# Kernel tuning notes

Hardware: AMD Instinct MI355X
Metric: run time of the kernel (lower is better)

Reference implementation:

```python
import jax, jax.numpy as jnp
import numpy as np

B = 256          # number of trees
DEPTH = 8        # complete binary tree depth -> 9 levels
M = 2 ** (DEPTH + 1) - 1   # 511 nodes per tree
N = B * M        # 130816 total nodes
X_SIZE = 128
H_SIZE = 128


def _build_forest():
    j = np.arange(M)
    parent_local = np.maximum((j - 1) // 2, 0)
    lvl = np.array([int(x + 1).bit_length() - 1 for x in j], dtype=np.int32)
    off = (np.arange(B) * M).astype(np.int32)
    parent = (parent_local[None, :] + off[:, None]).reshape(-1).astype(np.int32)
    level = np.tile(lvl, B)
    tree_id = np.repeat(np.arange(B, dtype=np.int32), M)
    isleaf = (level == DEPTH)
    jj = j[1:]
    edge_src = (jj[None, :] + off[:, None]).reshape(-1).astype(np.int32)   # child
    edge_dst = parent[edge_src]                                            # parent
    return parent, level, tree_id, isleaf, edge_src, edge_dst, off


def setup_inputs() -> dict:
    key = jax.random.key(0)
    ks = jax.random.split(key, 12)
    _, level, tree_id, isleaf, edge_src, edge_dst, root_ids = _build_forest()
    sx = 1.0 / np.sqrt(X_SIZE)
    sh = 1.0 / np.sqrt(H_SIZE)
    sxh = 1.0 / np.sqrt(X_SIZE + H_SIZE)
    inp = {
        "X": jax.random.normal(ks[0], (N, X_SIZE), dtype=jnp.float32),
        "h0": jnp.zeros((N, H_SIZE), jnp.float32),
        "c0": jnp.zeros((N, H_SIZE), jnp.float32),
        # bottom-up cell params
        "W_iou_bu": jax.random.normal(ks[1], (3 * H_SIZE, X_SIZE), dtype=jnp.float32) * sx,
        "U_iou_bu": jax.random.normal(ks[2], (3 * H_SIZE, H_SIZE), dtype=jnp.float32) * sh,
        "b_iou_bu": jnp.zeros((1, 3 * H_SIZE), jnp.float32),
        "Uf_bu": jax.random.normal(ks[3], (H_SIZE, H_SIZE), dtype=jnp.float32) * sh,
        "bf_bu": jax.random.normal(ks[4], (H_SIZE,), dtype=jnp.float32) * sh,
        # top-down cell params (x_size = X_SIZE + H_SIZE)
        "W_iou_td": jax.random.normal(ks[5], (3 * H_SIZE, X_SIZE + H_SIZE), dtype=jnp.float32) * sxh,
        "U_iou_td": jax.random.normal(ks[6], (3 * H_SIZE, H_SIZE), dtype=jnp.float32) * sh,
        "b_iou_td": jnp.zeros((1, 3 * H_SIZE), jnp.float32),
        "Uf_td": jax.random.normal(ks[7], (H_SIZE, H_SIZE), dtype=jnp.float32) * sh,
        "bf_td": jax.random.normal(ks[8], (H_SIZE,), dtype=jnp.float32) * sh,
        # graph structure
        "edge_src": jnp.asarray(edge_src),
        "edge_dst": jnp.asarray(edge_dst),
        "level": jnp.asarray(level),
        "tree_id": jnp.asarray(tree_id),
        "isleaf": jnp.asarray(isleaf),
        "root_ids": jnp.asarray(root_ids),
    }
    return inp


def _propagate(X_in, W_iou, U_iou, b_iou, Uf, bf, src, dst, level, no_in, h0, c0, order):
    """Level-synchronous ChildSum TreeLSTM propagation (== dgl.prop_nodes_topo)."""
    n = X_in.shape[0]
    WX = X_in @ W_iou.T                                   # [N, 3H]
    h, c = h0, c0
    for t in order:
        h_src = h[src]                                    # [E, H] gather child/parent states
        c_src = c[src]
        h_tild = jax.ops.segment_sum(h_src, dst, num_segments=n)
        f = jax.nn.sigmoid(h_src @ Uf.T + bf)             # per-edge forget gate
        c_red = jax.ops.segment_sum(f * c_src, dst, num_segments=n)
        iou = WX + h_tild @ U_iou.T + b_iou
        i, o, u = jnp.split(iou, 3, axis=1)
        c_base = jnp.where(no_in[:, None], c0, c_red)     # frontier nodes with no in-edges keep init c
        c_new = jax.nn.sigmoid(i) * jnp.tanh(u) + c_base
        h_new = jax.nn.sigmoid(o) * jnp.tanh(c_new)
        m = (level == t)[:, None]                          # only commit current topological level
        h = jnp.where(m, h_new, h)
        c = jnp.where(m, c_new, c)
    return h


def reference(X, h0, c0, W_iou_bu, U_iou_bu, b_iou_bu, Uf_bu, bf_bu,
              W_iou_td, U_iou_td, b_iou_td, Uf_td, bf_td,
              edge_src, edge_dst, level, tree_id, isleaf, root_ids):
    # bottom-up: messages flow child -> parent, leaves first
    h_bu = _propagate(X, W_iou_bu, U_iou_bu, b_iou_bu, Uf_bu, bf_bu,
                      edge_src, edge_dst, level, isleaf, h0, c0,
                      order=range(DEPTH, -1, -1))
    # top-down: reversed edges, root first
    X_td = jnp.concatenate([X, h_bu], axis=1)
    h_td = _propagate(X_td, W_iou_td, U_iou_td, b_iou_td, Uf_td, bf_td,
                      edge_dst, edge_src, level, level == 0, h0, c0,
                      order=range(0, DEPTH + 1))
    root_h_bottom_up = h_bu[root_ids]                     # [B, H]
    leaf = isleaf.astype(h_td.dtype)
    sums = jax.ops.segment_sum(h_td * leaf[:, None], tree_id, num_segments=root_ids.shape[0])
    cnt = jax.ops.segment_sum(leaf, tree_id, num_segments=root_ids.shape[0])
    leaves_h_top_down = sums / cnt[:, None]               # per-tree mean over leaves
    return jnp.concatenate([root_h_bottom_up, leaves_h_top_down], axis=1)
```

## Files before the change

### kernel.cpp

```cpp
#include <hip/hip_runtime.h>
#include <cmath>

#define NTREE 256
#define MPT 511
#define NNODE (NTREE * MPT)
#define HS 128

typedef __bf16 bf16x8 __attribute__((ext_vector_type(8)));
typedef float  f32x4  __attribute__((ext_vector_type(4)));

__device__ __forceinline__ float sigf(float x) {
  float e = __builtin_amdgcn_exp2f(x * -1.44269504f);
  return __builtin_amdgcn_rcpf(1.0f + e);
}
__device__ __forceinline__ float tanh_fast(float x) {
  float e = __builtin_amdgcn_exp2f(x * -2.88539008f);
  return __builtin_amdgcn_rcpf(1.0f + e) * 2.0f - 1.0f;
}
__device__ __forceinline__ f32x4 mm(bf16x8 a, bf16x8 b, f32x4 c) {
  return __builtin_amdgcn_mfma_f32_16x16x32_bf16(a, b, c, 0, 0, 0);
}
__device__ __forceinline__ int swz(int row, int rb, int kb) { return row * rb + (kb ^ ((row & 7) << 4)); }
__device__ __forceinline__ void st8(char* s, int row, int rb, int chunk, bf16x8 v) {
  *reinterpret_cast<bf16x8*>(s + swz(row, rb, chunk * 16)) = v;
}
__device__ __forceinline__ bf16x8 ld8(const char* s, int row, int rb, int kb) {
  return *reinterpret_cast<const bf16x8*>(s + swz(row, rb, kb));
}
__device__ __forceinline__ bf16x8 g8(const __bf16* p) { return *reinterpret_cast<const bf16x8*>(p); }
__device__ __forceinline__ bf16x8 gx8(const float* p) {
  float4 v0 = reinterpret_cast<const float4*>(p)[0];
  float4 v1 = reinterpret_cast<const float4*>(p)[1];
  bf16x8 o;
  o[0] = (__bf16)v0.x; o[1] = (__bf16)v0.y; o[2] = (__bf16)v0.z; o[3] = (__bf16)v0.w;
  o[4] = (__bf16)v1.x; o[5] = (__bf16)v1.y; o[6] = (__bf16)v1.z; o[7] = (__bf16)v1.w;
  return o;
}
__device__ __forceinline__ void stbf(char* s, int row, int rb, int kbyte, float v) {
  *reinterpret_cast<__bf16*>(s + row * rb + (kbyte ^ ((row & 7) << 4))) = (__bf16)v;
}

template <int MODE, bool EPI>
__global__ void __launch_bounds__(512, 2)
level_big8(int t,
           const float*  __restrict__ Xf,
           const __bf16* __restrict__ W,
           const float*  __restrict__ bp,
           const __bf16* __restrict__ Uf,
           const float*  __restrict__ bf_,
           __bf16* __restrict__ h_bu,
           __bf16* __restrict__ h_td,
           float*  __restrict__ cws,
           float*  __restrict__ part)
{
  constexpr int KA = (MODE == 0) ? 128 : 384;
  constexpr int KS = KA / 32;
  constexpr int BK = (MODE == 3) ? 384 : 256;
  constexpr int RB = KA * 2;
  constexpr int HB = (MODE == 0) ? 0 : 512;
  constexpr bool LEAFOUT = (MODE == 3 && !EPI);

  __shared__ __align__(16) char sA[64 * RB];
  __shared__ int sG[64], sP[64];

  const int tid = threadIdx.x;
  const int w = tid >> 6, l = tid & 63, lr = l & 15, lk = l >> 4;
  const int ch = w * 16 + lr;

  if (tid < 64) {
    int v = blockIdx.x * 64 + tid;
    int b = v >> t;
    int j = (1 << t) - 1 + (v & ((1 << t) - 1));
    sG[tid] = b * MPT + j;
    sP[tid] = b * MPT + ((j - 1) >> 1);
  }
  __syncthreads();

  bf16x8 Wr[KS][3];
#pragma unroll
  for (int ks = 0; ks < KS; ++ks)
#pragma unroll
    for (int g2 = 0; g2 < 3; ++g2)
      Wr[ks][g2] = g8(W + (size_t)(g2 * 128 + ch) * BK + ks * 32 + lk * 8);

#pragma unroll
  for (int it = 0; it < 2; ++it) {
    int idx = tid + it * 512, n = idx >> 4, e = idx & 15;
    st8(sA, n, RB, e, gx8(Xf + (size_t)sG[n] * HS + e * 8));
  }
  if constexpr (MODE == 3) {
#pragma unroll
    for (int it = 0; it < 2; ++it) {
      int idx = tid + it * 512, n = idx >> 4, e = idx & 15;
      st8(sA, n, RB, 16 + e, g8(h_bu + (size_t)sG[n] * HS + e * 8));
    }
#pragma unroll
    for (int it = 0; it < 2; ++it) {
      int idx = tid + it * 512, n = idx >> 4, e = idx & 15;
      st8(sA, n, RB, 32 + e, g8(h_td + (size_t)sP[n] * HS + e * 8));
    }
  }
  __syncthreads();

  float cb[4][4];
  const float bia = bp[ch], boa = bp[ch + 128], bua = bp[ch + 256];
  float bfa = 0.0f;
  if constexpr (EPI) bfa = bf_[ch];
  if constexpr (MODE == 3) {
#pragma unroll
    for (int mf = 0; mf < 4; ++mf)
#pragma unroll
      for (int j = 0; j < 4; ++j)
        cb[mf][j] = cws[(size_t)sP[16 * mf + lk * 4 + j] * HS + ch];
  }

  f32x4 acc[3][4];
#pragma unroll
  for (int g2 = 0; g2 < 3; ++g2)
#pragma unroll
    for (int mf = 0; mf < 4; ++mf) acc[g2][mf] = 0.0f;

#pragma unroll
  for (int ks = 0; ks < KS; ++ks) {
    bf16x8 A0 = ld8(sA, lr,      RB, ks * 64 + lk * 16);
    bf16x8 A1 = ld8(sA, 16 + lr, RB, ks * 64 + lk * 16);
    bf16x8 A2 = ld8(sA, 32 + lr, RB, ks * 64 + lk * 16);
    bf16x8 A3 = ld8(sA, 48 + lr, RB, ks * 64 + lk * 16);
#pragma unroll
    for (int g2 = 0; g2 < 3; ++g2) {
      acc[g2][0] = mm(A0, Wr[ks][g2], acc[g2][0]);
      acc[g2][1] = mm(A1, Wr[ks][g2], acc[g2][1]);
      acc[g2][2] = mm(A2, Wr[ks][g2], acc[g2][2]);
      acc[g2][3] = mm(A3, Wr[ks][g2], acc[g2][3]);
    }
  }

  float cnv[4][4], hnv[4][4];
  float psum = 0.0f;
#pragma unroll
  for (int mf = 0; mf < 4; ++mf)
#pragma unroll
    for (int j = 0; j < 4; ++j) {
      const int nrow = 16 * mf + lk * 4 + j;
      float cbase = (MODE == 0) ? 0.0f : cb[mf][j];
      float cn = sigf(acc[0][mf][j] + bia) * tanh_fast(acc[2][mf][j] + bua) + cbase;
      float hn = sigf(acc[1][mf][j] + boa) * tanh_fast(cn);
      if constexpr (!LEAFOUT)
        ((MODE == 3) ? h_td : h_bu)[(size_t)sG[nrow] * HS + ch] = (__bf16)hn;
      if constexpr (EPI) { cnv[mf][j] = cn; hnv[mf][j] = hn; }
      if constexpr (LEAFOUT) psum += hn;
    }

  if constexpr (LEAFOUT) {
    float s = psum;
    s += __shfl_xor(s, 16);
    s += __shfl_xor(s, 32);
    if (lk == 0) part[(size_t)blockIdx.x * 128 + ch] = s;
  }

  if constexpr (EPI) {
    bf16x8 Uff[4];
#pragma unroll
    for (int ks = 0; ks < 4; ++ks)
      Uff[ks] = g8(Uf + (size_t)ch * HS + ks * 32 + lk * 8);
    __syncthreads();
#pragma unroll
    for (int mf = 0; mf < 4; ++mf)
#pragma unroll
      for (int j = 0; j < 4; ++j)
        stbf(sA, 16 * mf + lk * 4 + j, RB, HB + 2 * ch, hnv[mf][j]);
    __syncthreads();
    f32x4 fa[4];
#pragma unroll
    for (int mf = 0; mf < 4; ++mf) fa[mf] = 0.0f;
#pragma unroll
    for (int ks = 0; ks < 4; ++ks) {
      bf16x8 a0 = ld8(sA, lr,      RB, HB + ks * 64 + lk * 16);
      bf16x8 a1 = ld8(sA, 16 + lr, RB, HB + ks * 64 + lk * 16);
      bf16x8 a2 = ld8(sA, 32 + lr, RB, HB + ks * 64 + lk * 16);
      bf16x8 a3 = ld8(sA, 48 + lr, RB, HB + ks * 64 + lk * 16);
      fa[0] = mm(a0, Uff[ks], fa[0]);
      fa[1] = mm(a1, Uff[ks], fa[1]);
      fa[2] = mm(a2, Uff[ks], fa[2]);
      fa[3] = mm(a3, Uff[ks], fa[3]);
    }
#pragma unroll
    for (int mf = 0; mf < 4; ++mf)
#pragma unroll
      for (int p = 0; p < 2; ++p) {
        const int er = 16 * mf + lk * 4 + 2 * p;
        float f0 = sigf(fa[mf][2 * p]     + bfa) * cnv[mf][2 * p];
        float f1 = sigf(fa[mf][2 * p + 1] + bfa) * cnv[mf][2 * p + 1];
        const int gp = sP[er];
        cws[(size_t)gp * HS + ch] = f0 + f1;
        h_bu[(size_t)gp * HS + ch] = (__bf16)(hnv[mf][2 * p] + hnv[mf][2 * p + 1]);
      }
  }
}

template <int MODE>
__global__ void __launch_bounds__(256, 2)
level_big(int t,
          const float*  __restrict__ Xf,
          const __bf16* __restrict__ W,
          const float*  __restrict__ bp,
          const __bf16* __restrict__ Uf,
          const float*  __restrict__ bf_,
          __bf16* __restrict__ h_bu,
          __bf16* __restrict__ h_td,
          float*  __restrict__ cws)
{
  constexpr int KA = (MODE == 1) ? 256 : 384;
  constexpr int KS = KA / 32;
  constexpr int BK = (MODE == 3) ? 384 : 256;
  constexpr int RB = KA * 2;
  constexpr int HB = (MODE == 1) ? 256 : 512;

  __shared__ __align__(16) char sA[64 * RB];
  __shared__ int sG[64], sP[64];

  const int tid = threadIdx.x;
  const int w = tid >> 6, l = tid & 63, lr = l & 15, lk = l >> 4;

  if (tid < 64) {
    int v = blockIdx.x * 64 + tid;
    int b = v >> t;
    int j = (1 << t) - 1 + (v & ((1 << t) - 1));
    sG[tid] = b * MPT + j;
    sP[tid] = b * MPT + ((j - 1) >> 1);
  }
  __syncthreads();

#pragma unroll
  for (int it = 0; it < 4; ++it) {
    int idx = tid + it * 256, n = idx >> 4, e = idx & 15;
    st8(sA, n, RB, e, gx8(Xf + (size_t)sG[n] * HS + e * 8));
  }
#pragma unroll
  for (int it = 0; it < 4; ++it) {
    int idx = tid + it * 256, n = idx >> 4, e = idx & 15;
    st8(sA, n, RB, 16 + e, g8(h_bu + (size_t)sG[n] * HS + e * 8));
  }
  if constexpr (MODE == 3) {
#pragma unroll
    for (int it = 0; it < 4; ++it) {
      int idx = tid + it * 256, n = idx >> 4, e = idx & 15;
      st8(sA, n, RB, 32 + e, g8(h_td + (size_t)sP[n] * HS + e * 8));
    }
  }
  __syncthreads();

  float cb[2][4][4];
  float bia[2], boa[2], bua[2], bfa[2];
#pragma unroll
  for (int nf = 0; nf < 2; ++nf) {
    const int ch = w * 32 + nf * 16 + lr;
    bia[nf] = bp[ch]; boa[nf] = bp[ch + 128]; bua[nf] = bp[ch + 256];
    bfa[nf] = bf_[ch];
#pragma unroll
    for (int mf = 0; mf < 4; ++mf)
#pragma unroll
      for (int j = 0; j < 4; ++j) {
        const int nrow = 16 * mf + lk * 4 + j;
        const int src = (MODE == 1) ? sG[nrow] : sP[nrow];
        cb[nf][mf][j] = cws[(size_t)src * HS + ch];
      }
  }

  f32x4 acc[6][4];
#pragma unroll
  for (int p = 0; p < 6; ++p)
#pragma unroll
    for (int mf = 0; mf < 4; ++mf) acc[p][mf] = 0.0f;

  bf16x8 A0[4], A1[4], Bb[3][6];
  auto ldA = [&](int ks, bf16x8* Ad) {
#pragma unroll
    for (int mf = 0; mf < 4; ++mf) Ad[mf] = ld8(sA, mf * 16 + lr, RB, ks * 64 + lk * 16);
  };
  auto ldB = [&](int ks, int s) {
#pragma unroll
    for (int g2 = 0; g2 < 3; ++g2)
#pragma unroll
      for (int nf = 0; nf < 2; ++nf)
        Bb[s][g2 * 2 + nf] = g8(W + (size_t)(g2 * 128 + w * 32 + nf * 16 + lr) * BK + ks * 32 + lk * 8);
  };

  ldB(0, 0); ldA(0, A0); ldB(1, 1);
#pragma unroll
  for (int ks = 0; ks < KS; ++ks) {
    bf16x8* Ac = (ks & 1) ? A1 : A0;
    bf16x8* An = (ks & 1) ? A0 : A1;
    if (ks + 1 < KS) ldA(ks + 1, An);
    if (ks + 2 < KS) ldB(ks + 2, (ks + 2) % 3);
#pragma unroll
    for (int p = 0; p < 6; ++p)
#pragma unroll
      for (int mf = 0; mf < 4; ++mf) acc[p][mf] = mm(Ac[mf], Bb[ks % 3][p], acc[p][mf]);
  }

  bf16x8 Uff[8];
#pragma unroll
  for (int ks = 0; ks < 4; ++ks)
#pragma unroll
    for (int nf = 0; nf < 2; ++nf)
      Uff[ks * 2 + nf] = g8(Uf + (size_t)(w * 32 + nf * 16 + lr) * HS + ks * 32 + lk * 8);

  __bf16* hp = (MODE == 3) ? h_td : h_bu;
  float cnv[2][4][4], hnv[2][4][4];
#pragma unroll
  for (int nf = 0; nf < 2; ++nf) {
    const int ch = w * 32 + nf * 16 + lr;
#pragma unroll
    for (int mf = 0; mf < 4; ++mf)
#pragma unroll
      for (int j = 0; j < 4; ++j) {
        const int nrow = 16 * mf + lk * 4 + j;
        float cn = sigf(acc[nf][mf][j] + bia[nf]) * tanh_fast(acc[4 + nf][mf][j] + bua[nf]) + cb[nf][mf][j];
        float hn = sigf(acc[2 + nf][mf][j] + boa[nf]) * tanh_fast(cn);
        hp[(size_t)sG[nrow] * HS + ch] = (__bf16)hn;
        cnv[nf][mf][j] = cn; hnv[nf][mf][j] = hn;
      }
  }

  __syncthreads();
#pragma unroll
  for (int nf = 0; nf < 2; ++nf) {
    const int ch = w * 32 + nf * 16 + lr;
#pragma unroll
    for (int mf = 0; mf < 4; ++mf)
#pragma unroll
      for (int j = 0; j < 4; ++j)
        stbf(sA, 16 * mf + lk * 4 + j, RB, HB + 2 * ch, hnv[nf][mf][j]);
  }
  __syncthreads();
  f32x4 fa[4][2];
#pragma unroll
  for (int mf = 0; mf < 4; ++mf) { fa[mf][0] = 0.0f; fa[mf][1] = 0.0f; }
#pragma unroll
  for (int ks = 0; ks < 4; ++ks) {
    bf16x8 a0 = ld8(sA, lr,      RB, HB + ks * 64 + lk * 16);
    bf16x8 a1 = ld8(sA, 16 + lr, RB, HB + ks * 64 + lk * 16);
    bf16x8 a2 = ld8(sA, 32 + lr, RB, HB + ks * 64 + lk * 16);
    bf16x8 a3 = ld8(sA, 48 + lr, RB, HB + ks * 64 + lk * 16);
#pragma unroll
    for (int nf = 0; nf < 2; ++nf) {
      fa[0][nf] = mm(a0, Uff[ks * 2 + nf], fa[0][nf]);
      fa[1][nf] = mm(a1, Uff[ks * 2 + nf], fa[1][nf]);
      fa[2][nf] = mm(a2, Uff[ks * 2 + nf], fa[2][nf]);
      fa[3][nf] = mm(a3, Uff[ks * 2 + nf], fa[3][nf]);
    }
  }
#pragma unroll
  for (int nf = 0; nf < 2; ++nf) {
    const int ch = w * 32 + nf * 16 + lr;
    if constexpr (MODE == 3) {
#pragma unroll
      for (int mf = 0; mf < 4; ++mf)
#pragma unroll
        for (int j = 0; j < 4; ++j) {
          const int nrow = 16 * mf + lk * 4 + j;
          cws[(size_t)sG[nrow] * HS + ch] = sigf(fa[mf][nf][j] + bfa[nf]) * cnv[nf][mf][j];
        }
    } else {
#pragma unroll
      for (int mf = 0; mf < 4; ++mf)
#pragma unroll
        for (int p = 0; p < 2; ++p) {
          const int er = 16 * mf + lk * 4 + 2 * p;
          float f0 = sigf(fa[mf][nf][2 * p]     + bfa[nf]) * cnv[nf][mf][2 * p];
          float f1 = sigf(fa[mf][nf][2 * p + 1] + bfa[nf]) * cnv[nf][mf][2 * p + 1];
          const int gp = sP[er];
          cws[(size_t)gp * HS + ch] = f0 + f1;
          h_bu[(size_t)gp * HS + ch] = (__bf16)(hnv[nf][mf][2 * p] + hnv[nf][mf][2 * p + 1]);
        }
    }
  }
}

__global__ void __launch_bounds__(512, 2)
small_both(const float* __restrict__ Xf,
           const __bf16* __restrict__ Wbu, const float* __restrict__ bbu,
           const __bf16* __restrict__ Ufb, const float* __restrict__ bfb,
           const __bf16* __restrict__ Wtd, const float* __restrict__ btd,
           const __bf16* __restrict__ Uft, const float* __restrict__ bft,
           __bf16* __restrict__ h_bu, __bf16* __restrict__ h_td,
           float* __restrict__ cws)
{
  __shared__ __align__(16) char sX[31 * 256];
  __shared__ __align__(16) char sH[31 * 256];
  __shared__ __align__(16) char sT[16 * 256];
  __shared__ __align__(16) char sTd[15 * 256];
  __shared__ float sCr[16][128];
  __shared__ float sFc[16][128];

  const int tid = threadIdx.x, w = tid >> 6, l = tid & 63, lr = l & 15, lk = l >> 4;
  const int ch = w * 16 + lr;
  const size_t base = (size_t)blockIdx.x * MPT * HS;

  for (int idx = tid; idx < 31 * 16; idx += 512) {
    int n = idx >> 4, e = idx & 15;
    st8(sX, n, 256, e, gx8(Xf + base + (size_t)n * HS + e * 8));
  }
  if (tid < 256) { int n = tid >> 4, e = tid & 15;
    st8(sT, n, 256, e, g8(h_bu + base + (size_t)(15 + n) * HS + e * 8)); }
  { int n = tid >> 5, e = tid & 31;
    reinterpret_cast<float4*>(&sCr[n][0])[e] =
        reinterpret_cast<const float4*>(cws + base + (size_t)(15 + n) * HS)[e]; }
  for (int idx = tid; idx < 15 * 16; idx += 512)
    *reinterpret_cast<float4*>(sTd + idx * 16) = float4{0.f, 0.f, 0.f, 0.f};

  {
    const float bia = bbu[ch], boa = bbu[ch + 128], bua = bbu[ch + 256], bfa = bfb[ch];
    bf16x8 Wb[8][3], Uff[4];
#pragma unroll
    for (int ks = 0; ks < 8; ++ks)
#pragma unroll
      for (int g2 = 0; g2 < 3; ++g2)
        Wb[ks][g2] = g8(Wbu + (size_t)(g2 * 128 + ch) * 256 + ks * 32 + lk * 8);
#pragma unroll
    for (int ks = 0; ks < 4; ++ks)
      Uff[ks] = g8(Ufb + (size_t)ch * HS + ks * 32 + lk * 8);
    __syncthreads();

    for (int t = 4; t >= 0; --t) {
      const int cnt = 1 << t, j0 = cnt - 1;
      f32x4 acc0 = 0.0f, acc1 = 0.0f, acc2 = 0.0f;
      bf16x8 Aa[3];
      auto ldA = [&](int ks, int s) {
        const int kb = (ks & 3) * 64 + lk * 16;
        Aa[s] = (ks < 4) ? ld8(sX, j0 + lr, 256, kb) : ld8(sT, lr, 256, kb);
      };
      ldA(0, 0); ldA(1, 1);
#pragma unroll
      for (int ks = 0; ks < 8; ++ks) {
        if (ks + 2 < 8) ldA(ks + 2, (ks + 2) % 3);
        acc0 = mm(Aa[ks % 3], Wb[ks][0], acc0);
        acc1 = mm(Aa[ks % 3], Wb[ks][1], acc1);
        acc2 = mm(Aa[ks % 3], Wb[ks][2], acc2);
      }
      float cnv[4], hnv[4];
#pragma unroll
      for (int j = 0; j < 4; ++j) {
        const int r = lk * 4 + j;
        float cn = sigf(acc0[j] + bia) * tanh_fast(acc2[j] + bua) + sCr[r][ch];
        float hn = sigf(acc1[j] + boa) * tanh_fast(cn);
        cnv[j] = cn; hnv[j] = hn;
        if (r < cnt) stbf(sH, j0 + r, 256, 2 * ch, hn);
      }
      if (t == 0 && lk == 0) h_bu[base + ch] = (__bf16)hnv[0];
      __syncthreads();
      if (t > 0) {
        f32x4 fa = 0.0f;
#pragma unroll
        for (int ks = 0; ks < 4; ++ks)
          fa = mm(ld8(sH, j0 + lr, 256, ks * 64 + lk * 16), Uff[ks], fa);
#pragma unroll
        for (int p = 0; p < 2; ++p) {
          const int pr = lk * 2 + p;
          if (pr < (cnt >> 1)) {
            float f0 = sigf(fa[2 * p]     + bfa) * cnv[2 * p];
            float f1 = sigf(fa[2 * p + 1] + bfa) * cnv[2 * p + 1];
            sCr[pr][ch] = f0 + f1;
            stbf(sT, pr, 256, 2 * ch, hnv[2 * p] + hnv[2 * p + 1]);
          }
        }
      }
      __syncthreads();
    }
  }

  {
    const float bia = btd[ch], boa = btd[ch + 128], bua = btd[ch + 256], bfa = bft[ch];
    bf16x8 Wt[12][3], Uff[4];
#pragma unroll
    for (int ks = 0; ks < 12; ++ks)
#pragma unroll
      for (int g2 = 0; g2 < 3; ++g2)
        Wt[ks][g2] = g8(Wtd + (size_t)(g2 * 128 + ch) * 384 + ks * 32 + lk * 8);
#pragma unroll
    for (int ks = 0; ks < 4; ++ks)
      Uff[ks] = g8(Uft + (size_t)ch * HS + ks * 32 + lk * 8);

    for (int t = 0; t <= 4; ++t) {
      const int cnt = 1 << t, j0 = cnt - 1;
      f32x4 acc0 = 0.0f, acc1 = 0.0f, acc2 = 0.0f;
      bf16x8 Aa[3];
      auto ldA = [&](int ks, int s) {
        const int kb = (ks & 3) * 64 + lk * 16;
        if (ks < 4)      Aa[s] = ld8(sX, j0 + lr, 256, kb);
        else if (ks < 8) Aa[s] = ld8(sH, j0 + lr, 256, kb);
        else { int pr = (j0 + lr - 1) >> 1; pr = pr < 0 ? 0 : pr;
               Aa[s] = ld8(sTd, pr, 256, kb); }
      };
      ldA(0, 0); ldA(1, 1);
#pragma unroll
      for (int ks = 0; ks < 12; ++ks) {
        if (ks + 2 < 12) ldA(ks + 2, (ks + 2) % 3);
        acc0 = mm(Aa[ks % 3], Wt[ks][0], acc0);
        acc1 = mm(Aa[ks % 3], Wt[ks][1], acc1);
        acc2 = mm(Aa[ks % 3], Wt[ks][2], acc2);
      }
      float cnv[4], hnv[4];
#pragma unroll
      for (int j = 0; j < 4; ++j) {
        const int r = lk * 4 + j;
        float cbv = (t == 0) ? 0.0f : sFc[r >> 1][ch];
        float cn = sigf(acc0[j] + bia) * tanh_fast(acc2[j] + bua) + cbv;
        float hn = sigf(acc1[j] + boa) * tanh_fast(cn);
        cnv[j] = cn; hnv[j] = hn;
        stbf(sT, r, 256, 2 * ch, hn);
        if (r < cnt && j0 + r < 15) stbf(sTd, j0 + r, 256, 2 * ch, hn);
        if (t == 4) h_td[base + (size_t)(15 + r) * HS + ch] = (__bf16)hn;
      }
      __syncthreads();
      f32x4 fa = 0.0f;
#pragma unroll
      for (int ks = 0; ks < 4; ++ks)
        fa = mm(ld8(sT, lr, 256, ks * 64 + lk * 16), Uff[ks], fa);
#pragma unroll
      for (int j = 0; j < 4; ++j) {
        const int r = lk * 4 + j;
        float fcv = sigf(fa[j] + bfa) * cnv[j];
        if (r < cnt) {
          if (t < 4) sFc[r][ch] = fcv;
          else       cws[base + (size_t)(15 + r) * HS + ch] = fcv;
        }
      }
      __syncthreads();
    }
  }
}

__global__ void __launch_bounds__(256)
prep(const float* __restrict__ Wbu, const float* __restrict__ Ubu,
     const float* __restrict__ Wtd, const float* __restrict__ Utd,
     const float* __restrict__ Ufb, const float* __restrict__ Uft,
     __bf16* wbu, __bf16* wtd, __bf16* ufb, __bf16* uft)
{
  int i = blockIdx.x * 256 + threadIdx.x;
  if (i < 98304) {
    int r = i >> 8, c = i & 255;
    wbu[i] = (__bf16)(c < 128 ? Wbu[r * 128 + c] : Ubu[r * 128 + c - 128]);
  } else if (i < 245760) {
    int k = i - 98304; int r = k / 384, c = k - r * 384;
    wtd[k] = (__bf16)(c < 256 ? Wtd[r * 256 + c] : Utd[r * 128 + (c - 256)]);
  } else if (i < 262144) {
    int k = i - 245760; ufb[k] = (__bf16)Ufb[k];
  } else {
    int k = i - 262144; uft[k] = (__bf16)Uft[k];
  }
}

__global__ void __launch_bounds__(128)
finalize_kernel(const __bf16* __restrict__ h_bu, const float* __restrict__ part,
                float* __restrict__ out)
{
  int b = blockIdx.x, ch = threadIdx.x;
  out[(size_t)b * 256 + ch] = (float)h_bu[((size_t)b * MPT) * HS + ch];
  const float* pp = part + (size_t)b * 512 + ch;
  out[(size_t)b * 256 + 128 + ch] = (pp[0] + pp[128] + pp[256] + pp[384]) * (1.0f / 256.0f);
}

extern "C" void kernel_launch(void* const* d_in, const int* in_sizes, int n_in,
                              void* d_out, int out_size, void* d_ws, size_t ws_size,
                              hipStream_t stream) {
  const float* X     = (const float*)d_in[0];
  const float* W_bu  = (const float*)d_in[3];
  const float* U_bu  = (const float*)d_in[4];
  const float* b_bu  = (const float*)d_in[5];
  const float* Uf_bu = (const float*)d_in[6];
  const float* bf_bu = (const float*)d_in[7];
  const float* W_td  = (const float*)d_in[8];
  const float* U_td  = (const float*)d_in[9];
  const float* b_td  = (const float*)d_in[10];
  const float* Uf_td = (const float*)d_in[11];
  const float* bf_td = (const float*)d_in[12];

  char* p = (char*)d_ws;
  __bf16* wbu  = (__bf16*)p; p += (size_t)384 * 256 * 2;
  __bf16* wtd  = (__bf16*)p; p += (size_t)384 * 384 * 2;
  __bf16* ufb  = (__bf16*)p; p += (size_t)128 * 128 * 2;
  __bf16* uft  = (__bf16*)p; p += (size_t)128 * 128 * 2;
  __bf16* h_bu = (__bf16*)p; p += (size_t)NNODE * HS * 2;
  __bf16* h_td = (__bf16*)p; p += (size_t)NNODE * HS * 2;
  float*  cws  = (float*)p;  p += (size_t)NNODE * HS * 4;
  float*  part = (float*)p;

  prep<<<1088, 256, 0, stream>>>(W_bu, U_bu, W_td, U_td, Uf_bu, Uf_td, wbu, wtd, ufb, uft);

  level_big8<0, true><<<1024, 512, 0, stream>>>(8, X, wbu, b_bu, ufb, bf_bu, h_bu, h_td, cws, part);
  level_big<1><<<512, 256, 0, stream>>>(7, X, wbu, b_bu, ufb, bf_bu, h_bu, h_td, cws);
  level_big<1><<<256, 256, 0, stream>>>(6, X, wbu, b_bu, ufb, bf_bu, h_bu, h_td, cws);
  level_big<1><<<128, 256, 0, stream>>>(5, X, wbu, b_bu, ufb, bf_bu, h_bu, h_td, cws);

  small_both<<<256, 512, 0, stream>>>(X, wbu, b_bu, ufb, bf_bu,
                                      wtd, b_td, uft, bf_td, h_bu, h_td, cws);

  level_big<3><<<128, 256, 0, stream>>>(5, X, wtd, b_td, uft, bf_td, h_bu, h_td, cws);
  level_big<3><<<256, 256, 0, stream>>>(6, X, wtd, b_td, uft, bf_td, h_bu, h_td, cws);
  level_big<3><<<512, 256, 0, stream>>>(7, X, wtd, b_td, uft, bf_td, h_bu, h_td, cws);
  level_big8<3, false><<<1024, 512, 0, stream>>>(8, X, wtd, b_td, uft, bf_td, h_bu, h_td, cws, part);

  finalize_kernel<<<256, 128, 0, stream>>>(h_bu, part, (float*)d_out);
}
```

Baseline: 262.7 us.

## Fuse bottom two tree levels into single kernels for bottom-up and top-down passes

Bottom-up levels 8 and 7 are merged into one kernel per 32-node level-7 group. Each block computes 64 leaves, keeps the reduced child h and forget-gated c in shared memory, then runs level 7 from them. The top-down pass does the same in reverse: level 7 and then the leaves, with the level-7 h_td and forget contribution kept on chip and the leaf h_td never written out. This drops a kernel launch and the global round trips of intermediate h/c in each direction. Weights are now streamed with a 3-slot register ring instead of being preloaded whole, trading more global weight reads and a larger LDS footprint per block for fewer passes.

```diff
diff --git a/kernel.cpp b/kernel.cpp
--- a/kernel.cpp
+++ b/kernel.cpp
@@ -40,79 +40,46 @@
   *reinterpret_cast<__bf16*>(s + row * rb + (kbyte ^ ((row & 7) << 4))) = (__bf16)v;
 }
 
-template <int MODE, bool EPI>
 __global__ void __launch_bounds__(512, 2)
-level_big8(int t,
-           const float*  __restrict__ Xf,
-           const __bf16* __restrict__ W,
-           const float*  __restrict__ bp,
-           const __bf16* __restrict__ Uf,
-           const float*  __restrict__ bf_,
-           __bf16* __restrict__ h_bu,
-           __bf16* __restrict__ h_td,
-           float*  __restrict__ cws,
-           float*  __restrict__ part)
+bu_bottom(const float* __restrict__ Xf,
+          const __bf16* __restrict__ W, const float* __restrict__ bp,
+          const __bf16* __restrict__ Uf, const float* __restrict__ bf_,
+          __bf16* __restrict__ h_bu, float* __restrict__ cws)
 {
-  constexpr int KA = (MODE == 0) ? 128 : 384;
-  constexpr int KS = KA / 32;
-  constexpr int BK = (MODE == 3) ? 384 : 256;
-  constexpr int RB = KA * 2;
-  constexpr int HB = (MODE == 0) ? 0 : 512;
-  constexpr bool LEAFOUT = (MODE == 3 && !EPI);
-
-  __shared__ __align__(16) char sA[64 * RB];
-  __shared__ int sG[64], sP[64];
-
-  const int tid = threadIdx.x;
-  const int w = tid >> 6, l = tid & 63, lr = l & 15, lk = l >> 4;
+  __shared__ __align__(16) char sX8[64 * 256];
+  __shared__ __align__(16) char sX7[32 * 256];
+  __shared__ __align__(16) char sT [32 * 256];
+  __shared__ float sCr[32][128];
+
+  const int tid = threadIdx.x, w = tid >> 6, l = tid & 63, lr = l & 15, lk = l >> 4;
   const int ch = w * 16 + lr;
-
-  if (tid < 64) {
-    int v = blockIdx.x * 64 + tid;
-    int b = v >> t;
-    int j = (1 << t) - 1 + (v & ((1 << t) - 1));
-    sG[tid] = b * MPT + j;
-    sP[tid] = b * MPT + ((j - 1) >> 1);
-  }
-  __syncthreads();
-
-  bf16x8 Wr[KS][3];
-#pragma unroll
-  for (int ks = 0; ks < KS; ++ks)
-#pragma unroll
-    for (int g2 = 0; g2 < 3; ++g2)
-      Wr[ks][g2] = g8(W + (size_t)(g2 * 128 + ch) * BK + ks * 32 + lk * 8);
+  const int vb = blockIdx.x * 32;
+  const int b  = vb >> 7;
+  const int j7 = 127 + (vb & 127);
+  const size_t g7  = (size_t)b * MPT + j7;
+  const size_t gLf = (size_t)b * MPT + 2 * j7 + 1;
+  const size_t gp6 = (size_t)b * MPT + ((j7 - 1) >> 1);
 
 #pragma unroll
   for (int it = 0; it < 2; ++it) {
     int idx = tid + it * 512, n = idx >> 4, e = idx & 15;
-    st8(sA, n, RB, e, gx8(Xf + (size_t)sG[n] * HS + e * 8));
-  }
-  if constexpr (MODE == 3) {
-#pragma unroll
-    for (int it = 0; it < 2; ++it) {
-      int idx = tid + it * 512, n = idx >> 4, e = idx & 15;
-      st8(sA, n, RB, 16 + e, g8(h_bu + (size_t)sG[n] * HS + e * 8));
-    }
-#pragma unroll
-    for (int it = 0; it < 2; ++it) {
-      int idx = tid + it * 512, n = idx >> 4, e = idx & 15;
-      st8(sA, n, RB, 32 + e, g8(h_td + (size_t)sP[n] * HS + e * 8));
-    }
-  }
-  __syncthreads();
-
-  float cb[4][4];
-  const float bia = bp[ch], boa = bp[ch + 128], bua = bp[ch + 256];
-  float bfa = 0.0f;
-  if constexpr (EPI) bfa = bf_[ch];
-  if constexpr (MODE == 3) {
-#pragma unroll
-    for (int mf = 0; mf < 4; ++mf)
-#pragma unroll
-      for (int j = 0; j < 4; ++j)
-        cb[mf][j] = cws[(size_t)sP[16 * mf + lk * 4 + j] * HS + ch];
-  }
+    st8(sX8, n, 256, e, gx8(Xf + (gLf + n) * HS + e * 8));
+  }
+  { int n = tid >> 4, e = tid & 15;
+    st8(sX7, n, 256, e, gx8(Xf + (g7 + n) * HS + e * 8)); }
+
+  const float bia = bp[ch], boa = bp[ch + 128], bua = bp[ch + 256], bfa = bf_[ch];
+  bf16x8 Uff[4];
+#pragma unroll
+  for (int ks = 0; ks < 4; ++ks) Uff[ks] = g8(Uf + (size_t)ch * HS + ks * 32 + lk * 8);
+  __syncthreads();
+
+  bf16x8 Bb[3][3];
+  auto ldB = [&](int ks, int s) {
+#pragma unroll
+    for (int g2 = 0; g2 < 3; ++g2)
+      Bb[s][g2] = g8(W + (size_t)(g2 * 128 + ch) * 256 + ks * 32 + lk * 8);
+  };
 
   f32x4 acc[3][4];
 #pragma unroll
@@ -120,82 +87,267 @@
 #pragma unroll
     for (int mf = 0; mf < 4; ++mf) acc[g2][mf] = 0.0f;
 
-#pragma unroll
-  for (int ks = 0; ks < KS; ++ks) {
-    bf16x8 A0 = ld8(sA, lr,      RB, ks * 64 + lk * 16);
-    bf16x8 A1 = ld8(sA, 16 + lr, RB, ks * 64 + lk * 16);
-    bf16x8 A2 = ld8(sA, 32 + lr, RB, ks * 64 + lk * 16);
-    bf16x8 A3 = ld8(sA, 48 + lr, RB, ks * 64 + lk * 16);
+  ldB(0, 0); ldB(1, 1);
+#pragma unroll
+  for (int ks = 0; ks < 4; ++ks) {
+    if (ks + 2 < 4) ldB(ks + 2, (ks + 2) % 3);
+    const int kb = ks * 64 + lk * 16;
+    bf16x8 A0 = ld8(sX8, lr,      256, kb);
+    bf16x8 A1 = ld8(sX8, 16 + lr, 256, kb);
+    bf16x8 A2 = ld8(sX8, 32 + lr, 256, kb);
+    bf16x8 A3 = ld8(sX8, 48 + lr, 256, kb);
 #pragma unroll
     for (int g2 = 0; g2 < 3; ++g2) {
-      acc[g2][0] = mm(A0, Wr[ks][g2], acc[g2][0]);
-      acc[g2][1] = mm(A1, Wr[ks][g2], acc[g2][1]);
-      acc[g2][2] = mm(A2, Wr[ks][g2], acc[g2][2]);
-      acc[g2][3] = mm(A3, Wr[ks][g2], acc[g2][3]);
-    }
-  }
-
+      acc[g2][0] = mm(A0, Bb[ks % 3][g2], acc[g2][0]);
+      acc[g2][1] = mm(A1, Bb[ks % 3][g2], acc[g2][1]);
+      acc[g2][2] = mm(A2, Bb[ks % 3][g2], acc[g2][2]);
+      acc[g2][3] = mm(A3, Bb[ks % 3][g2], acc[g2][3]);
+    }
+  }
   float cnv[4][4], hnv[4][4];
-  float psum = 0.0f;
 #pragma unroll
   for (int mf = 0; mf < 4; ++mf)
 #pragma unroll
     for (int j = 0; j < 4; ++j) {
       const int nrow = 16 * mf + lk * 4 + j;
-      float cbase = (MODE == 0) ? 0.0f : cb[mf][j];
-      float cn = sigf(acc[0][mf][j] + bia) * tanh_fast(acc[2][mf][j] + bua) + cbase;
+      float cn = sigf(acc[0][mf][j] + bia) * tanh_fast(acc[2][mf][j] + bua);
       float hn = sigf(acc[1][mf][j] + boa) * tanh_fast(cn);
-      if constexpr (!LEAFOUT)
-        ((MODE == 3) ? h_td : h_bu)[(size_t)sG[nrow] * HS + ch] = (__bf16)hn;
-      if constexpr (EPI) { cnv[mf][j] = cn; hnv[mf][j] = hn; }
-      if constexpr (LEAFOUT) psum += hn;
-    }
-
-  if constexpr (LEAFOUT) {
-    float s = psum;
-    s += __shfl_xor(s, 16);
-    s += __shfl_xor(s, 32);
-    if (lk == 0) part[(size_t)blockIdx.x * 128 + ch] = s;
-  }
-
-  if constexpr (EPI) {
-    bf16x8 Uff[4];
-#pragma unroll
-    for (int ks = 0; ks < 4; ++ks)
-      Uff[ks] = g8(Uf + (size_t)ch * HS + ks * 32 + lk * 8);
-    __syncthreads();
-#pragma unroll
-    for (int mf = 0; mf < 4; ++mf)
-#pragma unroll
-      for (int j = 0; j < 4; ++j)
-        stbf(sA, 16 * mf + lk * 4 + j, RB, HB + 2 * ch, hnv[mf][j]);
-    __syncthreads();
+      cnv[mf][j] = cn; hnv[mf][j] = hn;
+      h_bu[(gLf + nrow) * HS + ch] = (__bf16)hn;
+    }
+  __syncthreads();
+#pragma unroll
+  for (int mf = 0; mf < 4; ++mf)
+#pragma unroll
+    for (int j = 0; j < 4; ++j)
+      stbf(sX8, 16 * mf + lk * 4 + j, 256, 2 * ch, hnv[mf][j]);
+  __syncthreads();
+  {
     f32x4 fa[4];
 #pragma unroll
     for (int mf = 0; mf < 4; ++mf) fa[mf] = 0.0f;
 #pragma unroll
     for (int ks = 0; ks < 4; ++ks) {
-      bf16x8 a0 = ld8(sA, lr,      RB, HB + ks * 64 + lk * 16);
-      bf16x8 a1 = ld8(sA, 16 + lr, RB, HB + ks * 64 + lk * 16);
-      bf16x8 a2 = ld8(sA, 32 + lr, RB, HB + ks * 64 + lk * 16);
-      bf16x8 a3 = ld8(sA, 48 + lr, RB, HB + ks * 64 + lk * 16);
-      fa[0] = mm(a0, Uff[ks], fa[0]);
-      fa[1] = mm(a1, Uff[ks], fa[1]);
-      fa[2] = mm(a2, Uff[ks], fa[2]);
-      fa[3] = mm(a3, Uff[ks], fa[3]);
+      const int kb = ks * 64 + lk * 16;
+      fa[0] = mm(ld8(sX8, lr,      256, kb), Uff[ks], fa[0]);
+      fa[1] = mm(ld8(sX8, 16 + lr, 256, kb), Uff[ks], fa[1]);
+      fa[2] = mm(ld8(sX8, 32 + lr, 256, kb), Uff[ks], fa[2]);
+      fa[3] = mm(ld8(sX8, 48 + lr, 256, kb), Uff[ks], fa[3]);
     }
 #pragma unroll
     for (int mf = 0; mf < 4; ++mf)
 #pragma unroll
       for (int p = 0; p < 2; ++p) {
         const int er = 16 * mf + lk * 4 + 2 * p;
+        const int pr = er >> 1;
         float f0 = sigf(fa[mf][2 * p]     + bfa) * cnv[mf][2 * p];
         float f1 = sigf(fa[mf][2 * p + 1] + bfa) * cnv[mf][2 * p + 1];
-        const int gp = sP[er];
-        cws[(size_t)gp * HS + ch] = f0 + f1;
-        h_bu[(size_t)gp * HS + ch] = (__bf16)(hnv[mf][2 * p] + hnv[mf][2 * p + 1]);
-      }
-  }
+        sCr[pr][ch] = f0 + f1;
+        stbf(sT, pr, 256, 2 * ch, hnv[mf][2 * p] + hnv[mf][2 * p + 1]);
+      }
+  }
+  __syncthreads();
+
+  f32x4 ac2[3][2];
+#pragma unroll
+  for (int g2 = 0; g2 < 3; ++g2) { ac2[g2][0] = 0.0f; ac2[g2][1] = 0.0f; }
+  ldB(0, 0); ldB(1, 1);
+#pragma unroll
+  for (int ks = 0; ks < 8; ++ks) {
+    if (ks + 2 < 8) ldB(ks + 2, (ks + 2) % 3);
+    const int kb = (ks & 3) * 64 + lk * 16;
+    bf16x8 A0 = (ks < 4) ? ld8(sX7, lr,      256, kb) : ld8(sT, lr,      256, kb);
+    bf16x8 A1 = (ks < 4) ? ld8(sX7, 16 + lr, 256, kb) : ld8(sT, 16 + lr, 256, kb);
+#pragma unroll
+    for (int g2 = 0; g2 < 3; ++g2) {
+      ac2[g2][0] = mm(A0, Bb[ks % 3][g2], ac2[g2][0]);
+      ac2[g2][1] = mm(A1, Bb[ks % 3][g2], ac2[g2][1]);
+    }
+  }
+  float cn2[2][4], hn2[2][4];
+#pragma unroll
+  for (int mf = 0; mf < 2; ++mf)
+#pragma unroll
+    for (int j = 0; j < 4; ++j) {
+      const int nr = 16 * mf + lk * 4 + j;
+      float cn = sigf(ac2[0][mf][j] + bia) * tanh_fast(ac2[2][mf][j] + bua) + sCr[nr][ch];
+      float hn = sigf(ac2[1][mf][j] + boa) * tanh_fast(cn);
+      cn2[mf][j] = cn; hn2[mf][j] = hn;
+      h_bu[(g7 + nr) * HS + ch] = (__bf16)hn;
+    }
+  __syncthreads();
+#pragma unroll
+  for (int mf = 0; mf < 2; ++mf)
+#pragma unroll
+    for (int j = 0; j < 4; ++j)
+      stbf(sX7, 16 * mf + lk * 4 + j, 256, 2 * ch, hn2[mf][j]);
+  __syncthreads();
+  {
+    f32x4 fb[2]; fb[0] = 0.0f; fb[1] = 0.0f;
+#pragma unroll
+    for (int ks = 0; ks < 4; ++ks) {
+      const int kb = ks * 64 + lk * 16;
+      fb[0] = mm(ld8(sX7, lr,      256, kb), Uff[ks], fb[0]);
+      fb[1] = mm(ld8(sX7, 16 + lr, 256, kb), Uff[ks], fb[1]);
+    }
+#pragma unroll
+    for (int mf = 0; mf < 2; ++mf)
+#pragma unroll
+      for (int p = 0; p < 2; ++p) {
+        const int er = 16 * mf + lk * 4 + 2 * p;
+        const size_t gp = gp6 + (er >> 1);
+        float f0 = sigf(fb[mf][2 * p]     + bfa) * cn2[mf][2 * p];
+        float f1 = sigf(fb[mf][2 * p + 1] + bfa) * cn2[mf][2 * p + 1];
+        cws[gp * HS + ch] = f0 + f1;
+        h_bu[gp * HS + ch] = (__bf16)(hn2[mf][2 * p] + hn2[mf][2 * p + 1]);
+      }
+  }
+}
+
+__global__ void __launch_bounds__(512, 2)
+td_bottom(const float* __restrict__ Xf,
+          const __bf16* __restrict__ W, const float* __restrict__ bp,
+          const __bf16* __restrict__ Uf, const float* __restrict__ bf_,
+          const __bf16* __restrict__ h_bu, const __bf16* __restrict__ h_td,
+          const float* __restrict__ cws, float* __restrict__ part)
+{
+  __shared__ __align__(16) char sA7[32 * 768];
+  __shared__ __align__(16) char sXH[64 * 512];
+  __shared__ __align__(16) char sTd[32 * 256];
+  __shared__ float sFc[32][128];
+
+  const int tid = threadIdx.x, w = tid >> 6, l = tid & 63, lr = l & 15, lk = l >> 4;
+  const int ch = w * 16 + lr;
+  const int vb = blockIdx.x * 32;
+  const int b  = vb >> 7;
+  const int j7 = 127 + (vb & 127);
+  const size_t g7  = (size_t)b * MPT + j7;
+  const size_t gLf = (size_t)b * MPT + 2 * j7 + 1;
+  const size_t gp6 = (size_t)b * MPT + ((j7 - 1) >> 1);
+
+  { int n = tid >> 4, e = tid & 15;
+    st8(sA7, n, 768, e,      gx8(Xf   + (g7 + n) * HS + e * 8));
+    st8(sA7, n, 768, 16 + e, g8(h_bu + (g7 + n) * HS + e * 8));
+    st8(sA7, n, 768, 32 + e, g8(h_td + (gp6 + (n >> 1)) * HS + e * 8)); }
+#pragma unroll
+  for (int it = 0; it < 2; ++it) {
+    int idx = tid + it * 512, n = idx >> 4, e = idx & 15;
+    st8(sXH, n, 512, e,      gx8(Xf   + (gLf + n) * HS + e * 8));
+    st8(sXH, n, 512, 16 + e, g8(h_bu + (gLf + n) * HS + e * 8));
+  }
+  float cb[2][4];
+#pragma unroll
+  for (int mf = 0; mf < 2; ++mf)
+#pragma unroll
+    for (int j = 0; j < 4; ++j) {
+      const int nr = 16 * mf + lk * 4 + j;
+      cb[mf][j] = cws[(gp6 + (nr >> 1)) * HS + ch];
+    }
+  const float bia = bp[ch], boa = bp[ch + 128], bua = bp[ch + 256], bfa = bf_[ch];
+  bf16x8 Uff[4];
+#pragma unroll
+  for (int ks = 0; ks < 4; ++ks) Uff[ks] = g8(Uf + (size_t)ch * HS + ks * 32 + lk * 8);
+  __syncthreads();
+
+  bf16x8 Bb[3][3];
+  auto ldB = [&](int ks, int s) {
+#pragma unroll
+    for (int g2 = 0; g2 < 3; ++g2)
+      Bb[s][g2] = g8(W + (size_t)(g2 * 128 + ch) * 384 + ks * 32 + lk * 8);
+  };
+
+  f32x4 ac[3][2];
+#pragma unroll
+  for (int g2 = 0; g2 < 3; ++g2) { ac[g2][0] = 0.0f; ac[g2][1] = 0.0f; }
+  ldB(0, 0); ldB(1, 1);
+#pragma unroll
+  for (int ks = 0; ks < 12; ++ks) {
+    if (ks + 2 < 12) ldB(ks + 2, (ks + 2) % 3);
+    const int kb = ks * 64 + lk * 16;
+    bf16x8 A0 = ld8(sA7, lr,      768, kb);
+    bf16x8 A1 = ld8(sA7, 16 + lr, 768, kb);
+#pragma unroll
+    for (int g2 = 0; g2 < 3; ++g2) {
+      ac[g2][0] = mm(A0, Bb[ks % 3][g2], ac[g2][0]);
+      ac[g2][1] = mm(A1, Bb[ks % 3][g2], ac[g2][1]);
+    }
+  }
+  float cn7[2][4];
+#pragma unroll
+  for (int mf = 0; mf < 2; ++mf)
+#pragma unroll
+    for (int j = 0; j < 4; ++j) {
+      const int nr = 16 * mf + lk * 4 + j;
+      float cn = sigf(ac[0][mf][j] + bia) * tanh_fast(ac[2][mf][j] + bua) + cb[mf][j];
+      float hn = sigf(ac[1][mf][j] + boa) * tanh_fast(cn);
+      cn7[mf][j] = cn;
+      stbf(sTd, nr, 256, 2 * ch, hn);
+    }
+  __syncthreads();
+  {
+    f32x4 fa[2]; fa[0] = 0.0f; fa[1] = 0.0f;
+#pragma unroll
+    for (int ks = 0; ks < 4; ++ks) {
+      const int kb = ks * 64 + lk * 16;
+      fa[0] = mm(ld8(sTd, lr,      256, kb), Uff[ks], fa[0]);
+      fa[1] = mm(ld8(sTd, 16 + lr, 256, kb), Uff[ks], fa[1]);
+    }
+#pragma unroll
+    for (int mf = 0; mf < 2; ++mf)
+#pragma unroll
+      for (int j = 0; j < 4; ++j) {
+        const int nr = 16 * mf + lk * 4 + j;
+        sFc[nr][ch] = sigf(fa[mf][j] + bfa) * cn7[mf][j];
+      }
+  }
+  __syncthreads();
+
+  f32x4 a8[3][4];
+#pragma unroll
+  for (int g2 = 0; g2 < 3; ++g2)
+#pragma unroll
+    for (int mf = 0; mf < 4; ++mf) a8[g2][mf] = 0.0f;
+  ldB(0, 0); ldB(1, 1);
+#pragma unroll
+  for (int ks = 0; ks < 12; ++ks) {
+    if (ks + 2 < 12) ldB(ks + 2, (ks + 2) % 3);
+    bf16x8 A0, A1, A2, A3;
+    if (ks < 8) {
+      const int kb = ks * 64 + lk * 16;
+      A0 = ld8(sXH, lr,      512, kb);
+      A1 = ld8(sXH, 16 + lr, 512, kb);
+      A2 = ld8(sXH, 32 + lr, 512, kb);
+      A3 = ld8(sXH, 48 + lr, 512, kb);
+    } else {
+      const int kb = (ks - 8) * 64 + lk * 16;
+      A0 = ld8(sTd, (lr >> 1),      256, kb);
+      A1 = ld8(sTd, 8 + (lr >> 1),  256, kb);
+      A2 = ld8(sTd, 16 + (lr >> 1), 256, kb);
+      A3 = ld8(sTd, 24 + (lr >> 1), 256, kb);
+    }
+#pragma unroll
+    for (int g2 = 0; g2 < 3; ++g2) {
+      a8[g2][0] = mm(A0, Bb[ks % 3][g2], a8[g2][0]);
+      a8[g2][1] = mm(A1, Bb[ks % 3][g2], a8[g2][1]);
+      a8[g2][2] = mm(A2, Bb[ks % 3][g2], a8[g2][2]);
+      a8[g2][3] = mm(A3, Bb[ks % 3][g2], a8[g2][3]);
+    }
+  }
+  float psum = 0.0f;
+#pragma unroll
+  for (int mf = 0; mf < 4; ++mf)
+#pragma unroll
+    for (int j = 0; j < 4; ++j) {
+      const int nrow = 16 * mf + lk * 4 + j;
+      float cbase = sFc[nrow >> 1][ch];
+      float cn = sigf(a8[0][mf][j] + bia) * tanh_fast(a8[2][mf][j] + bua) + cbase;
+      float hn = sigf(a8[1][mf][j] + boa) * tanh_fast(cn);
+      psum += hn;
+    }
+  float s = psum;
+  s += __shfl_xor(s, 16);
+  s += __shfl_xor(s, 32);
+  if (lk == 0) part[(size_t)blockIdx.x * 128 + ch] = s;
 }
 
 template <int MODE>
@@ -589,8 +741,7 @@
 
   prep<<<1088, 256, 0, stream>>>(W_bu, U_bu, W_td, U_td, Uf_bu, Uf_td, wbu, wtd, ufb, uft);
 
-  level_big8<0, true><<<1024, 512, 0, stream>>>(8, X, wbu, b_bu, ufb, bf_bu, h_bu, h_td, cws, part);
-  level_big<1><<<512, 256, 0, stream>>>(7, X, wbu, b_bu, ufb, bf_bu, h_bu, h_td, cws);
+  bu_bottom<<<1024, 512, 0, stream>>>(X, wbu, b_bu, ufb, bf_bu, h_bu, cws);
   level_big<1><<<256, 256, 0, stream>>>(6, X, wbu, b_bu, ufb, bf_bu, h_bu, h_td, cws);
   level_big<1><<<128, 256, 0, stream>>>(5, X, wbu, b_bu, ufb, bf_bu, h_bu, h_td, cws);
 
@@ -599,8 +750,7 @@
 
   level_big<3><<<128, 256, 0, stream>>>(5, X, wtd, b_td, uft, bf_td, h_bu, h_td, cws);
   level_big<3><<<256, 256, 0, stream>>>(6, X, wtd, b_td, uft, bf_td, h_bu, h_td, cws);
-  level_big<3><<<512, 256, 0, stream>>>(7, X, wtd, b_td, uft, bf_td, h_bu, h_td, cws);
-  level_big8<3, false><<<1024, 512, 0, stream>>>(8, X, wtd, b_td, uft, bf_td, h_bu, h_td, cws, part);
+  td_bottom<<<1024, 512, 0, stream>>>(X, wtd, b_td, uft, bf_td, h_bu, h_td, cws, part);
 
   finalize_kernel<<<256, 128, 0, stream>>>(h_bu, part, (float*)d_out);
 }
```

Result: no change. 260.1 us (-1.0%).
